# Optimization experiments

Hardware: AMD Instinct MI355X
Metric: run time of the kernel (lower is better)

The kernel has to match this reference:

```python
import jax, jax.numpy as jnp
import numpy as np

DEGREE = 3


def get_knot_vector(n_cp, degree):
    # Clamped uniform knot vector of length n_cp + degree + 1 (static numpy).
    p = degree
    if n_cp - p - 1 > 0:
        internal = np.linspace(0.0, 1.0, n_cp - p + 1)[1:-1]
        knots = np.concatenate([np.zeros(p + 1), internal, np.ones(p + 1)])
    else:
        knots = np.concatenate([np.zeros(p + 1), np.ones(p + 1)])
    return jnp.asarray(knots, dtype=jnp.float32)


def bspline_basis(t, knots, degree, n_cp):
    # Degree-0 indicators, vectorized over control-point index i. [n_cp, num_points]
    left = knots[:n_cp]
    right = knots[1:n_cp + 1]
    N = ((t[None, :] >= left[:, None]) & (t[None, :] < right[:, None])).astype(t.dtype)
    # Last interval is closed on the right.
    N = N.at[-1].set(((t >= left[-1]) & (t <= right[-1])).astype(t.dtype))
    # Cox-de Boor recursion over degree (small static loop).
    for d in range(1, degree + 1):
        d1 = knots[d:d + n_cp] - knots[:n_cp]            # knots[i+d]-knots[i]
        d2 = knots[d + 1:d + 1 + n_cp] - knots[1:1 + n_cp]  # knots[i+d+1]-knots[i+1]
        s1 = jnp.where(d1 != 0, d1, 1.0)
        s2 = jnp.where(d2 != 0, d2, 1.0)
        term1 = jnp.where(d1[:, None] != 0,
                          (t[None, :] - knots[:n_cp, None]) / s1[:, None] * N, 0.0)
        N_shift = jnp.concatenate([N[1:], jnp.zeros((1, N.shape[1]), N.dtype)], axis=0)
        term2 = jnp.where(d2[:, None] != 0,
                          (knots[d + 1:d + 1 + n_cp, None] - t[None, :]) / s2[:, None] * N_shift,
                          0.0)
        N = term1 + term2
    return N


def setup_inputs() -> dict:
    key = jax.random.key(0)
    k1, k2, k3, k4 = jax.random.split(key, 4)
    B, n_cp = 2048, 32
    return {
        "bspline_cp": jax.random.normal(k1, (B, n_cp, 2), dtype=jnp.float32),
        "nurbs_cp": jax.random.normal(k2, (B, n_cp, 2), dtype=jnp.float32),
        "nurbs_weights": jax.random.uniform(k3, (B, n_cp), dtype=jnp.float32),
        "bezier_cp": jax.random.normal(k4, (B, n_cp, 2), dtype=jnp.float32),
        "num_points": 2048,
    }


def reference(bspline_cp, nurbs_cp, nurbs_weights, bezier_cp, num_points):
    p = DEGREE
    B, n_cp, _ = bspline_cp.shape
    knots = get_knot_vector(n_cp, p)
    t = jnp.linspace(knots[p], knots[-p - 1], num_points)
    basis = bspline_basis(t, knots, p, n_cp)  # [n_cp, num_points]

    # B-spline curve: [B, 2, num_points]
    bspline_curve = jnp.einsum('in,bid->bdn', basis, bspline_cp)

    # Bezier (Bernstein) curve, vectorized over control-point index.
    n_bez = bezier_cp.shape[1] - 1
    tb = jnp.linspace(0.0, 1.0, num_points)
    i = jnp.arange(n_bez + 1, dtype=jnp.float32)
    coeff = jnp.exp(jax.scipy.special.gammaln(n_bez + 1.0)
                    - jax.scipy.special.gammaln(i + 1.0)
                    - jax.scipy.special.gammaln(n_bez - i + 1.0))
    # bernstein: [num_points, n_bez+1]
    bern = coeff[None, :] * tb[:, None] ** i[None, :] * (1.0 - tb[:, None]) ** (n_bez - i)[None, :]
    bezier_curve = jnp.einsum('ni,bid->bdn', bern, bezier_cp)  # [B, 2, num_points]

    # NURBS curve: [B, 2, num_points]
    weighted_basis = nurbs_weights[:, :, None] * basis[None, :, :]  # [B, n_cp, num_points]
    numerator = jnp.einsum('bin,bij->bjn', weighted_basis, nurbs_cp)
    denominator = weighted_basis.sum(axis=1, keepdims=True)
    nurbs_curve = numerator / (denominator + 1e-8)

    return bspline_curve, nurbs_curve, bezier_curve
```

## Files before the change

kernel.cpp:

```cpp
#include <hip/hip_runtime.h>

#define NPTS 2048
#define NCP  32
#define P    4
#define GB   2

static __device__ const float C31[NCP] = {
    1.f, 31.f, 465.f, 4495.f, 31465.f, 169911.f, 736281.f, 2629575.f,
    7888725.f, 20160075.f, 44352165.f, 84672315.f, 141120525.f, 206253075.f,
    265182525.f, 300540195.f, 300540195.f, 265182525.f, 206253075.f, 141120525.f,
    84672315.f, 44352165.f, 20160075.f, 7888725.f, 2629575.f, 736281.f,
    169911.f, 31465.f, 4495.f, 465.f, 31.f, 1.f
};

__device__ __forceinline__ float knq(int i) {
    int m = i - 3;
    m = m < 0 ? 0 : m;
    return (m >= 29) ? 1.0f : (float)m * (float)(1.0 / 29.0);
}

__global__ void __launch_bounds__(256, 6) fused_kernel(
    const float* __restrict__ bspline_cp, const float* __restrict__ nurbs_cp,
    const float* __restrict__ nurbs_w, const float* __restrict__ bezier_cp,
    float* __restrict__ out, int B) {
    const int tid = threadIdx.x;
    const int n0  = (blockIdx.x * 256 + tid) * P;
    const int b0  = blockIdx.y * GB;

    __shared__ float s_bs[GB * NCP * 2];
    __shared__ float s_nc[GB * NCP * 2];
    __shared__ float s_bz[GB * NCP * 2];
    __shared__ float s_w [GB * NCP];
    if (tid < GB * NCP * 2) {
        s_bs[tid] = bspline_cp[(size_t)b0 * NCP * 2 + tid];
        s_nc[tid] = nurbs_cp [(size_t)b0 * NCP * 2 + tid];
        s_bz[tid] = bezier_cp[(size_t)b0 * NCP * 2 + tid];
    }
    if (tid < GB * NCP)
        s_w[tid] = nurbs_w[(size_t)b0 * NCP + tid];
    __syncthreads();

    const unsigned cs = (unsigned)B * 2u * NPTS;

    float tt[P];
    int   sp_[P];
    float bv[P][4];
#pragma unroll
    for (int p = 0; p < P; ++p) {
        const float t = (float)((double)(n0 + p) * (1.0 / (double)(NPTS - 1)));
        tt[p] = t;
        int s = (int)(t * 29.0f);
        s = s < 28 ? s : 28;
        sp_[p] = s;
        const int j = s + 3;
        const float L1 = t - knq(j);
        const float R1 = knq(j + 1) - t;
        const float L2 = t - knq(j - 1);
        const float R2 = knq(j + 2) - t;
        const float L3 = t - knq(j - 2);
        const float R3 = knq(j + 3) - t;
        float N0, N1, N2, N3, tmp, sv;
        tmp = __builtin_amdgcn_rcpf(R1 + L1);
        N0 = R1 * tmp;
        N1 = L1 * tmp;
        tmp = N0 * __builtin_amdgcn_rcpf(R1 + L2);
        N0 = R1 * tmp;
        sv = L2 * tmp;
        tmp = N1 * __builtin_amdgcn_rcpf(R2 + L1);
        N1 = fmaf(R2, tmp, sv);
        N2 = L1 * tmp;
        tmp = N0 * __builtin_amdgcn_rcpf(R1 + L3);
        N0 = R1 * tmp;
        sv = L3 * tmp;
        tmp = N1 * __builtin_amdgcn_rcpf(R2 + L2);
        N1 = fmaf(R2, tmp, sv);
        sv = L2 * tmp;
        tmp = N2 * __builtin_amdgcn_rcpf(R3 + L1);
        N2 = fmaf(R3, tmp, sv);
        N3 = L1 * tmp;
        bv[p][0] = N0; bv[p][1] = N1; bv[p][2] = N2; bv[p][3] = N3;
    }

#pragma unroll
    for (int g = 0; g < GB; ++g) {
        float obx[P], oby[P], onx[P], ony[P];
#pragma unroll
        for (int p = 0; p < P; ++p) {
            float sbx = 0.f, sby = 0.f, snx = 0.f, sny = 0.f, den = 0.f;
#pragma unroll
            for (int k = 0; k < 4; ++k) {
                const int idx = sp_[p] + k;
                const float c = bv[p][k];
                float2 cb = *reinterpret_cast<const float2*>(&s_bs[g * 64 + idx * 2]);
                sbx = fmaf(c, cb.x, sbx); sby = fmaf(c, cb.y, sby);
                const float wb = c * s_w[g * 32 + idx];
                den += wb;
                float2 cn = *reinterpret_cast<const float2*>(&s_nc[g * 64 + idx * 2]);
                snx = fmaf(wb, cn.x, snx); sny = fmaf(wb, cn.y, sny);
            }
            const float inv = __builtin_amdgcn_rcpf(den + 1e-8f);
            obx[p] = sbx; oby[p] = sby;
            onx[p] = snx * inv; ony[p] = sny * inv;
        }
        const unsigned base = (unsigned)(b0 + g) * 2u * NPTS + (unsigned)n0;
        *reinterpret_cast<float4*>(&out[base]) =
            make_float4(obx[0], obx[1], obx[2], obx[3]);
        *reinterpret_cast<float4*>(&out[base + NPTS]) =
            make_float4(oby[0], oby[1], oby[2], oby[3]);
        *reinterpret_cast<float4*>(&out[cs + base]) =
            make_float4(onx[0], onx[1], onx[2], onx[3]);
        *reinterpret_cast<float4*>(&out[cs + base + NPTS]) =
            make_float4(ony[0], ony[1], ony[2], ony[3]);
    }

    float dd[P], e0[P];
#pragma unroll
    for (int p = 0; p < P; ++p) {
        const float lu = __builtin_amdgcn_logf(fmaxf(tt[p], 1e-30f));
        const float lv = __builtin_amdgcn_logf(fmaxf(1.0f - tt[p], 1e-30f));
        dd[p] = lu - lv;
        e0[p] = 31.0f * lv;
    }
    float ex[GB][P], ey[GB][P];
#pragma unroll
    for (int g = 0; g < GB; ++g)
#pragma unroll
        for (int p = 0; p < P; ++p) { ex[g][p] = 0.f; ey[g][p] = 0.f; }
#pragma unroll
    for (int i = 0; i < NCP; i += 2) {
        float ba[P], bb[P];
#pragma unroll
        for (int p = 0; p < P; ++p) {
            ba[p] = C31[i]     * __builtin_amdgcn_exp2f(fmaf((float)i,       dd[p], e0[p]));
            bb[p] = C31[i + 1] * __builtin_amdgcn_exp2f(fmaf((float)(i + 1), dd[p], e0[p]));
        }
#pragma unroll
        for (int g = 0; g < GB; ++g) {
            float4 c = *reinterpret_cast<const float4*>(&s_bz[g * 64 + 2 * i]);
#pragma unroll
            for (int p = 0; p < P; ++p) {
                ex[g][p] = fmaf(ba[p], c.x, fmaf(bb[p], c.z, ex[g][p]));
                ey[g][p] = fmaf(ba[p], c.y, fmaf(bb[p], c.w, ey[g][p]));
            }
        }
    }
#pragma unroll
    for (int g = 0; g < GB; ++g) {
        const unsigned base = 2u * cs + (unsigned)(b0 + g) * 2u * NPTS + (unsigned)n0;
        *reinterpret_cast<float4*>(&out[base]) =
            make_float4(ex[g][0], ex[g][1], ex[g][2], ex[g][3]);
        *reinterpret_cast<float4*>(&out[base + NPTS]) =
            make_float4(ey[g][0], ey[g][1], ey[g][2], ey[g][3]);
    }
}

extern "C" void kernel_launch(void* const* d_in, const int* in_sizes, int n_in,
                              void* d_out, int out_size, void* d_ws, size_t ws_size,
                              hipStream_t stream) {
    const float* bspline_cp = (const float*)d_in[0];
    const float* nurbs_cp   = (const float*)d_in[1];
    const float* nurbs_w    = (const float*)d_in[2];
    const float* bezier_cp  = (const float*)d_in[3];
    float* out = (float*)d_out;

    const int B = in_sizes[2] / NCP;

    hipLaunchKernelGGL(fused_kernel, dim3(NPTS / (256 * P), B / GB), dim3(256), 0, stream,
                       bspline_cp, nurbs_cp, nurbs_w, bezier_cp, out, B);
}
```

Before: 32.88 us.

## Process one batch per block with interleaved float4 control-point layout

Drops the two-batches-per-block grouping, so each block handles a single batch row and the grid doubles in y. The basis evaluation and the B-spline/NURBS accumulation are fused into one loop, and the B-spline and NURBS control points are interleaved into one float4 shared array so each point needs one LDS read. Launch bounds rise to 8 waves per SIMD to raise occupancy. In exchange, the Bernstein exp2 and log work and the basis setup are no longer shared across two batches, so total transcendental work per output roughly doubles.

```diff
diff --git a/kernel.cpp b/kernel.cpp
--- a/kernel.cpp
+++ b/kernel.cpp
@@ -3,7 +3,6 @@
 #define NPTS 2048
 #define NCP  32
 #define P    4
-#define GB   2
 
 static __device__ const float C31[NCP] = {
     1.f, 31.f, 465.f, 4495.f, 31465.f, 169911.f, 736281.f, 2629575.f,
@@ -19,39 +18,38 @@
     return (m >= 29) ? 1.0f : (float)m * (float)(1.0 / 29.0);
 }
 
-__global__ void __launch_bounds__(256, 6) fused_kernel(
+__global__ void __launch_bounds__(256, 8) fused_kernel(
     const float* __restrict__ bspline_cp, const float* __restrict__ nurbs_cp,
     const float* __restrict__ nurbs_w, const float* __restrict__ bezier_cp,
     float* __restrict__ out, int B) {
     const int tid = threadIdx.x;
     const int n0  = (blockIdx.x * 256 + tid) * P;
-    const int b0  = blockIdx.y * GB;
+    const int b   = blockIdx.y;
 
-    __shared__ float s_bs[GB * NCP * 2];
-    __shared__ float s_nc[GB * NCP * 2];
-    __shared__ float s_bz[GB * NCP * 2];
-    __shared__ float s_w [GB * NCP];
-    if (tid < GB * NCP * 2) {
-        s_bs[tid] = bspline_cp[(size_t)b0 * NCP * 2 + tid];
-        s_nc[tid] = nurbs_cp [(size_t)b0 * NCP * 2 + tid];
-        s_bz[tid] = bezier_cp[(size_t)b0 * NCP * 2 + tid];
+    __shared__ float4 s_cpn[NCP];
+    __shared__ float  s_bz[NCP * 2];
+    __shared__ float  s_w [NCP];
+    if (tid < 128) {
+        const int i = tid >> 2, c = tid & 3;
+        const float* src = (c < 2) ? bspline_cp : nurbs_cp;
+        reinterpret_cast<float*>(s_cpn)[tid] = src[(size_t)b * 64 + i * 2 + (c & 1)];
+    } else if (tid < 192) {
+        s_bz[tid - 128] = bezier_cp[(size_t)b * 64 + (tid - 128)];
+    } else if (tid < 224) {
+        s_w[tid - 192] = nurbs_w[(size_t)b * 32 + (tid - 192)];
     }
-    if (tid < GB * NCP)
-        s_w[tid] = nurbs_w[(size_t)b0 * NCP + tid];
     __syncthreads();
 
     const unsigned cs = (unsigned)B * 2u * NPTS;
 
     float tt[P];
-    int   sp_[P];
-    float bv[P][4];
+    float obx[P], oby[P], onx[P], ony[P];
 #pragma unroll
     for (int p = 0; p < P; ++p) {
         const float t = (float)((double)(n0 + p) * (1.0 / (double)(NPTS - 1)));
         tt[p] = t;
         int s = (int)(t * 29.0f);
         s = s < 28 ? s : 28;
-        sp_[p] = s;
         const int j = s + 3;
         const float L1 = t - knq(j);
         const float R1 = knq(j + 1) - t;
@@ -78,31 +76,24 @@
         tmp = N2 * __builtin_amdgcn_rcpf(R3 + L1);
         N2 = fmaf(R3, tmp, sv);
         N3 = L1 * tmp;
-        bv[p][0] = N0; bv[p][1] = N1; bv[p][2] = N2; bv[p][3] = N3;
+
+        float sbx = 0.f, sby = 0.f, snx = 0.f, sny = 0.f, den = 0.f;
+#pragma unroll
+        for (int k = 0; k < 4; ++k) {
+            const int idx = s + k;
+            const float c = (k == 0) ? N0 : (k == 1) ? N1 : (k == 2) ? N2 : N3;
+            const float4 q = s_cpn[idx];
+            sbx = fmaf(c, q.x, sbx); sby = fmaf(c, q.y, sby);
+            const float wb = c * s_w[idx];
+            den += wb;
+            snx = fmaf(wb, q.z, snx); sny = fmaf(wb, q.w, sny);
+        }
+        const float inv = __builtin_amdgcn_rcpf(den + 1e-8f);
+        obx[p] = sbx; oby[p] = sby;
+        onx[p] = snx * inv; ony[p] = sny * inv;
     }
-
-#pragma unroll
-    for (int g = 0; g < GB; ++g) {
-        float obx[P], oby[P], onx[P], ony[P];
-#pragma unroll
-        for (int p = 0; p < P; ++p) {
-            float sbx = 0.f, sby = 0.f, snx = 0.f, sny = 0.f, den = 0.f;
-#pragma unroll
-            for (int k = 0; k < 4; ++k) {
-                const int idx = sp_[p] + k;
-                const float c = bv[p][k];
-                float2 cb = *reinterpret_cast<const float2*>(&s_bs[g * 64 + idx * 2]);
-                sbx = fmaf(c, cb.x, sbx); sby = fmaf(c, cb.y, sby);
-                const float wb = c * s_w[g * 32 + idx];
-                den += wb;
-                float2 cn = *reinterpret_cast<const float2*>(&s_nc[g * 64 + idx * 2]);
-                snx = fmaf(wb, cn.x, snx); sny = fmaf(wb, cn.y, sny);
-            }
-            const float inv = __builtin_amdgcn_rcpf(den + 1e-8f);
-            obx[p] = sbx; oby[p] = sby;
-            onx[p] = snx * inv; ony[p] = sny * inv;
-        }
-        const unsigned base = (unsigned)(b0 + g) * 2u * NPTS + (unsigned)n0;
+    {
+        const unsigned base = (unsigned)b * 2u * NPTS + (unsigned)n0;
         *reinterpret_cast<float4*>(&out[base]) =
             make_float4(obx[0], obx[1], obx[2], obx[3]);
         *reinterpret_cast<float4*>(&out[base + NPTS]) =
@@ -121,11 +112,9 @@
         dd[p] = lu - lv;
         e0[p] = 31.0f * lv;
     }
-    float ex[GB][P], ey[GB][P];
+    float ex[P], ey[P];
 #pragma unroll
-    for (int g = 0; g < GB; ++g)
-#pragma unroll
-        for (int p = 0; p < P; ++p) { ex[g][p] = 0.f; ey[g][p] = 0.f; }
+    for (int p = 0; p < P; ++p) { ex[p] = 0.f; ey[p] = 0.f; }
 #pragma unroll
     for (int i = 0; i < NCP; i += 2) {
         float ba[P], bb[P];
@@ -134,23 +123,19 @@
             ba[p] = C31[i]     * __builtin_amdgcn_exp2f(fmaf((float)i,       dd[p], e0[p]));
             bb[p] = C31[i + 1] * __builtin_amdgcn_exp2f(fmaf((float)(i + 1), dd[p], e0[p]));
         }
+        const float4 c = *reinterpret_cast<const float4*>(&s_bz[2 * i]);
 #pragma unroll
-        for (int g = 0; g < GB; ++g) {
-            float4 c = *reinterpret_cast<const float4*>(&s_bz[g * 64 + 2 * i]);
-#pragma unroll
-            for (int p = 0; p < P; ++p) {
-                ex[g][p] = fmaf(ba[p], c.x, fmaf(bb[p], c.z, ex[g][p]));
-                ey[g][p] = fmaf(ba[p], c.y, fmaf(bb[p], c.w, ey[g][p]));
-            }
+        for (int p = 0; p < P; ++p) {
+            ex[p] = fmaf(ba[p], c.x, fmaf(bb[p], c.z, ex[p]));
+            ey[p] = fmaf(ba[p], c.y, fmaf(bb[p], c.w, ey[p]));
         }
     }
-#pragma unroll
-    for (int g = 0; g < GB; ++g) {
-        const unsigned base = 2u * cs + (unsigned)(b0 + g) * 2u * NPTS + (unsigned)n0;
+    {
+        const unsigned base = 2u * cs + (unsigned)b * 2u * NPTS + (unsigned)n0;
         *reinterpret_cast<float4*>(&out[base]) =
-            make_float4(ex[g][0], ex[g][1], ex[g][2], ex[g][3]);
+            make_float4(ex[0], ex[1], ex[2], ex[3]);
         *reinterpret_cast<float4*>(&out[base + NPTS]) =
-            make_float4(ey[g][0], ey[g][1], ey[g][2], ey[g][3]);
+            make_float4(ey[0], ey[1], ey[2], ey[3]);
     }
 }
 
@@ -165,6 +150,6 @@
 
     const int B = in_sizes[2] / NCP;
 
-    hipLaunchKernelGGL(fused_kernel, dim3(NPTS / (256 * P), B / GB), dim3(256), 0, stream,
+    hipLaunchKernelGGL(fused_kernel, dim3(NPTS / (256 * P), B), dim3(256), 0, stream,
                        bspline_cp, nurbs_cp, nurbs_w, bezier_cp, out, B);
 }
```

After: 90.79 us. 176% more time.
